# Kernel optimization log

Measured on AMD Instinct MI355X. Metric: run time of the kernel, lower is better.

The kernel has to match this reference:

```python
import jax, jax.numpy as jnp
import numpy as np
from jax import lax

# LNS semantics: values are held as (sign, log_base|x|); exact conversion round-trips
# make log-domain mul/add mathematically identical to float conv/linear/relu, so the
# faithful reference is the equivalent float pipeline.

def _conv(x, w, b):
    # x: [B,C,H,W], w: [O,C,kh,kw] (torch layout), stride 1, no padding
    y = lax.conv_general_dilated(x, w, window_strides=(1, 1), padding='VALID',
                                 dimension_numbers=('NCHW', 'OIHW', 'NCHW'))
    return y + b[None, :, None, None]

def _maxpool2(x):
    return lax.reduce_window(x, -jnp.inf, lax.max,
                             window_dimensions=(1, 1, 2, 2),
                             window_strides=(1, 1, 2, 2), padding='VALID')

def setup_inputs() -> dict:
    key = jax.random.key(0)
    ks = jax.random.split(key, 9)
    s = lambda k, shape, fan: jax.random.normal(k, shape, jnp.float32) * (1.0 / np.sqrt(fan))
    return {
        'x': jax.random.normal(ks[0], (512, 1, 54, 54), jnp.float32),
        'conv1_w': s(ks[1], (32, 1, 3, 3), 9),
        'conv1_b': s(ks[2], (32,), 9),
        'conv2_w': s(ks[3], (64, 32, 3, 3), 32 * 9),
        'conv2_b': s(ks[4], (64,), 32 * 9),
        'fc1_w': s(ks[5], (128, 9216), 9216),
        'fc1_b': s(ks[6], (128,), 9216),
        'fc2_w': s(ks[7], (10, 128), 128),
        'fc2_b': s(ks[8], (10,), 128),
    }

def reference(x, conv1_w, conv1_b, conv2_w, conv2_b, fc1_w, fc1_b, fc2_w, fc2_b):
    h = jnp.maximum(_conv(x, conv1_w, conv1_b), 0.0)          # [B,32,52,52]
    h = _maxpool2(h)                                          # [B,32,26,26]
    h = jnp.maximum(_conv(h, conv2_w, conv2_b), 0.0)          # [B,64,24,24]
    h = _maxpool2(h)                                          # [B,64,12,12]
    h = h.reshape(h.shape[0], -1)                             # [B,9216]
    h = jnp.maximum(h @ fc1_w.T + fc1_b, 0.0)                 # [B,128]
    return h @ fc2_w.T + fc2_b                                # [B,10]
```

## Files before the change

### kernel.cpp

```cpp
#include <hip/hip_runtime.h>


#define B 512
#define POS 676
#define ICP 36
#define P2SZ (64*12*12)
#define SCR 26
#define IMS 58
#define IMCOPY (54 * IMS)
#define PL_USH (POS * ICP)
#define SCRATCH_USH 6656

typedef unsigned short ushort_t;
typedef ushort_t ushort4v __attribute__((ext_vector_type(4)));
typedef _Float16 f16x8 __attribute__((ext_vector_type(8)));
typedef float f32x4 __attribute__((ext_vector_type(4)));

__device__ __forceinline__ ushort_t f2h(float f) {
    union { _Float16 h; ushort_t u; } a; a.h = (_Float16)f; return a.u;
}
__device__ __forceinline__ float h2f(ushort_t u) {
    union { ushort_t u; _Float16 h; } a; a.u = u; return (float)a.h;
}

#define N_WR (64 * 9 * 32)
#define WR_BLOCKS 72
#define TR_BLOCKS 128
#define PREP_THREADS ((WR_BLOCKS + TR_BLOCKS) * 256)

__global__ __launch_bounds__(256) void prep(const float* __restrict__ c2w,
                                            const float* __restrict__ f1w,
                                            ushort_t* __restrict__ wr,
                                            ushort_t* __restrict__ wfb,
                                            float* __restrict__ C) {
    __shared__ float tr[64 * 145];
    int blk = blockIdx.x;
    int tid = threadIdx.x;

    int gtid = blk * 256 + tid;
    for (int i = gtid; i < 512 * 128; i += PREP_THREADS) C[i] = 0.0f;

    if (blk < WR_BLOCKS) {
        int t = blk * 256 + tid;
        int ic  = t & 31;
        int tap = (t >> 5) % 9;
        int oc  = t / 288;
        wr[t] = f2h(c2w[oc * 288 + ic * 9 + tap]);
        return;
    }
    int n = blk - WR_BLOCKS;
    const float* src = f1w + (size_t)n * 9216;
#pragma unroll
    for (int i = 0; i < 36; ++i) {
        int idx = i * 256 + tid;
        int oc = idx / 144, pos = idx - oc * 144;
        tr[oc * 145 + pos] = src[idx];
    }
    __syncthreads();
    ushort_t* dst = wfb + (size_t)n * 9216;
#pragma unroll
    for (int i = 0; i < 36; ++i) {
        int idx = i * 256 + tid;
        int pos = idx >> 6, oc = idx & 63;
        dst[idx] = f2h(tr[oc * 145 + pos]);
    }
}

__global__ __launch_bounds__(512, 4) void conv12(const float* __restrict__ x,
                                                 const float* __restrict__ w1,
                                                 const float* __restrict__ bias1,
                                                 const ushort_t* __restrict__ wr,
                                                 const float* __restrict__ bias2,
                                                 ushort_t* __restrict__ pool2cl) {
    __shared__ ushort_t smem[PL_USH + SCRATCH_USH];
    ushort_t* pl  = smem;
    ushort_t* img = smem + PL_USH;

    int b   = blockIdx.x;
    int tid = threadIdx.x;
    int lane = tid & 63, wid = tid >> 6;
    int quad = lane >> 4, lr = lane & 15;

    for (int i = tid; i < 54; i += 512) {
        ushort_t* r0 = img + i * IMS;
        r0[54] = 0; r0[55] = 0; r0[56] = 0; r0[57] = 0;
        ushort_t* r1 = img + IMCOPY + i * IMS;
        r1[53] = 0; r1[54] = 0; r1[55] = 0; r1[56] = 0; r1[57] = 0;
    }
    if (tid < 96) img[2 * IMCOPY + tid] = 0;

    const float* xim = x + (size_t)b * 2916;
    for (int i = tid; i < 729; i += 512) {
        int e = i * 4;
        int r = e / 54, c = e - r * 54;
        float4 xv = *reinterpret_cast<const float4*>(&xim[e]);
        ushort_t h0 = f2h(xv.x), h1 = f2h(xv.y), h2 = f2h(xv.z), h3 = f2h(xv.w);
        if (c <= 50) {
            ushort_t* p0 = &img[r * IMS + c];
            p0[0] = h0; p0[1] = h1; p0[2] = h2; p0[3] = h3;
            ushort_t* p1 = &img[IMCOPY + r * IMS + c - 1];
            if (c > 0) p1[0] = h0;
            p1[1] = h1; p1[2] = h2; p1[3] = h3;
        } else {
            img[r * IMS + 52] = h0;
            img[r * IMS + 53] = h1;
            img[(r + 1) * IMS + 0] = h2;
            img[(r + 1) * IMS + 1] = h3;
            img[IMCOPY + r * IMS + 51] = h0;
            img[IMCOPY + r * IMS + 52] = h1;
            img[IMCOPY + (r + 1) * IMS + 0] = h3;
        }
    }

    f16x8 bfrag[2];
#pragma unroll
    for (int n = 0; n < 2; ++n) {
        union { ushort_t u[8]; f16x8 v; } bu;
#pragma unroll
        for (int j = 0; j < 8; ++j) bu.u[j] = 0;
        if (quad < 3) {
            const float* wp = w1 + (n * 16 + lr) * 9 + quad * 3;
            bu.u[0] = f2h(wp[0]);
            bu.u[1] = f2h(wp[1]);
            bu.u[2] = f2h(wp[2]);
        }
        bfrag[n] = bu.v;
    }
    float bv0 = bias1[lr], bv1 = bias1[16 + lr];

    __syncthreads();

    int cbase = (lr & 1) ? (IMCOPY + lr - 1) : lr;

    for (int it = 0; it < 4; ++it) {
        int py = wid + it * 8;
        if (py >= 26) break;
        int y0 = 2 * py;
#pragma unroll
        for (int t = 0; t < 4; ++t) {
            int x0 = t * 16;
            int off0 = cbase + x0 + (y0 + quad) * IMS;
            int off1 = off0 + IMS;
            union { unsigned d[4]; f16x8 v; } a0, a1;
            a0.d[0] = *reinterpret_cast<const unsigned*>(&img[off0]);
            a0.d[1] = *reinterpret_cast<const unsigned*>(&img[off0 + 2]);
            a0.d[2] = a0.d[0]; a0.d[3] = a0.d[1];
            a1.d[0] = *reinterpret_cast<const unsigned*>(&img[off1]);
            a1.d[1] = *reinterpret_cast<const unsigned*>(&img[off1 + 2]);
            a1.d[2] = a1.d[0]; a1.d[3] = a1.d[1];

            f32x4 cA0 = (f32x4){0.f,0.f,0.f,0.f}, cA1 = cA0, cB0 = cA0, cB1 = cA0;
            cA0 = __builtin_amdgcn_mfma_f32_16x16x32_f16(a0.v, bfrag[0], cA0, 0, 0, 0);
            cA1 = __builtin_amdgcn_mfma_f32_16x16x32_f16(a0.v, bfrag[1], cA1, 0, 0, 0);
            cB0 = __builtin_amdgcn_mfma_f32_16x16x32_f16(a1.v, bfrag[0], cB0, 0, 0, 0);
            cB1 = __builtin_amdgcn_mfma_f32_16x16x32_f16(a1.v, bfrag[1], cB1, 0, 0, 0);

            if (t < 3 || quad == 0) {
                int px0 = t * 8 + quad * 2;
                float u0 = fmaxf(fmaxf(cA0[0], cA0[1]), fmaxf(cB0[0], cB0[1]));
                float u1 = fmaxf(fmaxf(cA0[2], cA0[3]), fmaxf(cB0[2], cB0[3]));
                float v0 = fmaxf(fmaxf(cA1[0], cA1[1]), fmaxf(cB1[0], cB1[1]));
                float v1 = fmaxf(fmaxf(cA1[2], cA1[3]), fmaxf(cB1[2], cB1[3]));
                ushort_t* po = pl + (py * 26 + px0) * ICP;
                po[lr]            = f2h(fmaxf(u0 + bv0, 0.0f));
                po[16 + lr]       = f2h(fmaxf(v0 + bv1, 0.0f));
                po[ICP + lr]      = f2h(fmaxf(u1 + bv0, 0.0f));
                po[ICP + 16 + lr] = f2h(fmaxf(v1 + bv1, 0.0f));
            }
        }
    }

    __syncthreads();

    int prow  = wid >> 1;
    int nhalf = wid & 1;
    const ushort_t* wb = wr + (size_t)(nhalf * 32 + lr) * 288 + quad * 8;

    int ocl = lane & 31;
    int pxh = lane >> 5;
    int oc  = nhalf * 32 + ocl;
    float bv = bias2[oc];
    ushort_t* scr = smem + PL_USH + wid * (32 * SCR);

    for (int cc = 0; cc < 3; ++cc) {
        int ebase[3];
#pragma unroll
        for (int t = 0; t < 3; ++t) {
            int m  = t * 16 + lr;
            int yl = m / 24;
            int xx = m - yl * 24;
            ebase[t] = ((8 * cc + 2 * prow + yl) * 26 + xx) * ICP + quad * 8;
        }

        f32x4 acc[3][2];
#pragma unroll
        for (int t = 0; t < 3; ++t)
#pragma unroll
            for (int n = 0; n < 2; ++n) acc[t][n] = (f32x4){0.f, 0.f, 0.f, 0.f};

#pragma unroll
        for (int tap = 0; tap < 9; ++tap) {
            int ky = tap / 3, kx = tap % 3;
            int koff = (ky * 26 + kx) * ICP;
            f16x8 a[3];
#pragma unroll
            for (int t = 0; t < 3; ++t) {
                union { ushort4v s[2]; f16x8 v; } u;
                u.s[0] = *reinterpret_cast<const ushort4v*>(&pl[ebase[t] + koff]);
                u.s[1] = *reinterpret_cast<const ushort4v*>(&pl[ebase[t] + koff + 4]);
                a[t] = u.v;
            }
            f16x8 bf[2];
#pragma unroll
            for (int n = 0; n < 2; ++n)
                bf[n] = *reinterpret_cast<const f16x8*>(wb + (size_t)n * 16 * 288 + tap * 32);
#pragma unroll
            for (int t = 0; t < 3; ++t)
#pragma unroll
                for (int n = 0; n < 2; ++n)
                    acc[t][n] = __builtin_amdgcn_mfma_f32_16x16x32_f16(a[t], bf[n], acc[t][n], 0, 0, 0);
        }

#pragma unroll
        for (int t = 0; t < 3; ++t)
#pragma unroll
            for (int n = 0; n < 2; ++n) {
                int wocl = n * 16 + lr;
                int i0 = t * 8 + quad * 2;
                float v0 = fmaxf(acc[t][n][0], acc[t][n][1]);
                float v1 = fmaxf(acc[t][n][2], acc[t][n][3]);
                union { ushort_t u2[2]; unsigned w; } pk;
                pk.u2[0] = f2h(v0); pk.u2[1] = f2h(v1);
                *reinterpret_cast<unsigned*>(&scr[wocl * SCR + i0]) = pk.w;
            }
        asm volatile("s_waitcnt lgkmcnt(0)" ::: "memory");

        const ushort_t* row = scr + ocl * SCR;
        int py = cc * 4 + prow;
        ushort_t* po = pool2cl + ((size_t)b * 144 + py * 12) * 64 + oc;
#pragma unroll
        for (int j = 0; j < 6; ++j) {
            int px = pxh * 6 + j;
            float r0 = h2f(row[px]);
            float r1 = h2f(row[px + 12]);
            po[px * 64] = f2h(fmaxf(fmaxf(r0, r1) + bv, 0.0f));
        }
        asm volatile("s_waitcnt lgkmcnt(0)" ::: "memory");
    }
}

__global__ __launch_bounds__(256) void fc1_mfma(const ushort_t* __restrict__ A,
                                                 const ushort_t* __restrict__ W,
                                                 float* __restrict__ C) {
    int tid = threadIdx.x;
    int lane = tid & 63, wid = tid >> 6;
    int lr = lane & 15, quad = lane >> 4;
    int w  = blockIdx.x * 4 + wid;
    int nt = w & 3;
    int ks = (w >> 2) & 15;
    int mt = w >> 6;

    int m0 = mt * 16;
    int n0 = nt * 32;
    int k0 = ks * 576 + quad * 8;
    const ushort_t* a0 = A + (size_t)(m0 + lr) * 9216 + k0;
    const ushort_t* b0 = W + (size_t)(n0 + lr) * 9216 + k0;
    const ushort_t* b1 = b0 + (size_t)16 * 9216;

    f32x4 acc0 = (f32x4){0.f, 0.f, 0.f, 0.f};
    f32x4 acc1 = (f32x4){0.f, 0.f, 0.f, 0.f};

#pragma unroll
    for (int kk = 0; kk < 18; ++kk) {
        f16x8 av  = *reinterpret_cast<const f16x8*>(a0 + kk * 32);
        f16x8 bv0 = *reinterpret_cast<const f16x8*>(b0 + kk * 32);
        f16x8 bv1 = *reinterpret_cast<const f16x8*>(b1 + kk * 32);
        acc0 = __builtin_amdgcn_mfma_f32_16x16x32_f16(av, bv0, acc0, 0, 0, 0);
        acc1 = __builtin_amdgcn_mfma_f32_16x16x32_f16(av, bv1, acc1, 0, 0, 0);
    }

    int crow = m0 + quad * 4;
#pragma unroll
    for (int r = 0; r < 4; ++r) {
        atomicAdd(&C[(size_t)(crow + r) * 128 + n0 + lr],      acc0[r]);
        atomicAdd(&C[(size_t)(crow + r) * 128 + n0 + 16 + lr], acc1[r]);
    }
}

__global__ __launch_bounds__(256) void fc2k(const float* __restrict__ C,
                                            const float* __restrict__ b1,
                                            const float* __restrict__ w2,
                                            const float* __restrict__ b2,
                                            float* __restrict__ out) {
    __shared__ float h[2][128];
    int half = threadIdx.x >> 7;
    int k = threadIdx.x & 127;
    int b = blockIdx.x * 2 + half;
    float s = C[(size_t)b * 128 + k];
    h[half][k] = fmaxf(s + b1[k], 0.0f);
    __syncthreads();
    if (k < 10) {
        const float* wp = w2 + k * 128;
        float acc = 0.f;
#pragma unroll 8
        for (int j = 0; j < 128; ++j) acc += h[half][j] * wp[j];
        out[b * 10 + k] = acc + b2[k];
    }
}

extern "C" void kernel_launch(void* const* d_in, const int* in_sizes, int n_in,
                              void* d_out, int out_size, void* d_ws, size_t ws_size,
                              hipStream_t stream) {
    const float* x       = (const float*)d_in[0];
    const float* conv1_w = (const float*)d_in[1];
    const float* conv1_b = (const float*)d_in[2];
    const float* conv2_w = (const float*)d_in[3];
    const float* conv2_b = (const float*)d_in[4];
    const float* fc1_w   = (const float*)d_in[5];
    const float* fc1_b   = (const float*)d_in[6];
    const float* fc2_w   = (const float*)d_in[7];
    const float* fc2_b   = (const float*)d_in[8];
    float* out = (float*)d_out;

    char* ws = (char*)d_ws;
    ushort_t* wr = (ushort_t*)ws;
    ws += N_WR * sizeof(ushort_t) + 128;
    ushort_t* wfb = (ushort_t*)ws;
    ws += (size_t)128 * 9216 * sizeof(ushort_t) + 128;
    ushort_t* pool2cl = (ushort_t*)ws;
    ws += (size_t)B * P2SZ * sizeof(ushort_t) + 128;
    float* C = (float*)ws;
    ws += (size_t)512 * 128 * sizeof(float) + 128;

    prep<<<WR_BLOCKS + TR_BLOCKS, 256, 0, stream>>>(conv2_w, fc1_w, wr, wfb, C);
    conv12<<<B, 512, 0, stream>>>(x, conv1_w, conv1_b, wr, conv2_b, pool2cl);
    fc1_mfma<<<512, 256, 0, stream>>>(pool2cl, wfb, C);
    fc2k<<<256, 256, 0, stream>>>(C, fc1_b, fc2_w, fc2_b, out);
}
```

Measured before the change: 114.6 us.

## Fuse fc2 into fc1 via last-block counter and widen fc1 M tile

Each fc1 wave now computes a 32x32 output tile with four MFMA accumulators, halving the block count and reusing the weight loads across two row tiles. A global atomic counter, zeroed in prep, detects the last finishing block, which then applies bias and ReLU and computes the fc2 layer for all rows. This removes the separate fc2 kernel launch. The cost is a serial single-block epilogue at the tail and less parallelism in fc1.

```diff
diff --git a/kernel.cpp b/kernel.cpp
--- a/kernel.cpp
+++ b/kernel.cpp
@@ -27,6 +27,7 @@
 #define WR_BLOCKS 72
 #define TR_BLOCKS 128
 #define PREP_THREADS ((WR_BLOCKS + TR_BLOCKS) * 256)
+#define FC1_BLOCKS 256
 
 __global__ __launch_bounds__(256) void prep(const float* __restrict__ c2w,
                                             const float* __restrict__ f1w,
@@ -38,7 +39,7 @@
     int tid = threadIdx.x;
 
     int gtid = blk * 256 + tid;
-    for (int i = gtid; i < 512 * 128; i += PREP_THREADS) C[i] = 0.0f;
+    for (int i = gtid; i < 512 * 128 + 16; i += PREP_THREADS) C[i] = 0.0f;
 
     if (blk < WR_BLOCKS) {
         int t = blk * 256 + tid;
@@ -250,8 +251,15 @@
 }
 
 __global__ __launch_bounds__(256) void fc1_mfma(const ushort_t* __restrict__ A,
-                                                 const ushort_t* __restrict__ W,
-                                                 float* __restrict__ C) {
+                                                const ushort_t* __restrict__ W,
+                                                float* __restrict__ C,
+                                                int* __restrict__ counter,
+                                                const float* __restrict__ fb1,
+                                                const float* __restrict__ w2,
+                                                const float* __restrict__ fb2,
+                                                float* __restrict__ out) {
+    __shared__ float w2s[10 * 128];
+    __shared__ int lastFlag;
     int tid = threadIdx.x;
     int lane = tid & 63, wid = tid >> 6;
     int lr = lane & 15, quad = lane >> 4;
@@ -260,51 +268,68 @@
     int ks = (w >> 2) & 15;
     int mt = w >> 6;
 
-    int m0 = mt * 16;
+    int m0 = mt * 32;
     int n0 = nt * 32;
     int k0 = ks * 576 + quad * 8;
-    const ushort_t* a0 = A + (size_t)(m0 + lr) * 9216 + k0;
-    const ushort_t* b0 = W + (size_t)(n0 + lr) * 9216 + k0;
-    const ushort_t* b1 = b0 + (size_t)16 * 9216;
-
-    f32x4 acc0 = (f32x4){0.f, 0.f, 0.f, 0.f};
-    f32x4 acc1 = (f32x4){0.f, 0.f, 0.f, 0.f};
+    const ushort_t* a0  = A + (size_t)(m0 + lr) * 9216 + k0;
+    const ushort_t* a1  = a0 + (size_t)16 * 9216;
+    const ushort_t* b0  = W + (size_t)(n0 + lr) * 9216 + k0;
+    const ushort_t* b1p = b0 + (size_t)16 * 9216;
+
+    f32x4 acc00 = (f32x4){0.f,0.f,0.f,0.f};
+    f32x4 acc01 = acc00, acc10 = acc00, acc11 = acc00;
 
 #pragma unroll
     for (int kk = 0; kk < 18; ++kk) {
-        f16x8 av  = *reinterpret_cast<const f16x8*>(a0 + kk * 32);
+        f16x8 av0 = *reinterpret_cast<const f16x8*>(a0 + kk * 32);
+        f16x8 av1 = *reinterpret_cast<const f16x8*>(a1 + kk * 32);
         f16x8 bv0 = *reinterpret_cast<const f16x8*>(b0 + kk * 32);
-        f16x8 bv1 = *reinterpret_cast<const f16x8*>(b1 + kk * 32);
-        acc0 = __builtin_amdgcn_mfma_f32_16x16x32_f16(av, bv0, acc0, 0, 0, 0);
-        acc1 = __builtin_amdgcn_mfma_f32_16x16x32_f16(av, bv1, acc1, 0, 0, 0);
+        f16x8 bv1 = *reinterpret_cast<const f16x8*>(b1p + kk * 32);
+        acc00 = __builtin_amdgcn_mfma_f32_16x16x32_f16(av0, bv0, acc00, 0, 0, 0);
+        acc01 = __builtin_amdgcn_mfma_f32_16x16x32_f16(av0, bv1, acc01, 0, 0, 0);
+        acc10 = __builtin_amdgcn_mfma_f32_16x16x32_f16(av1, bv0, acc10, 0, 0, 0);
+        acc11 = __builtin_amdgcn_mfma_f32_16x16x32_f16(av1, bv1, acc11, 0, 0, 0);
     }
 
     int crow = m0 + quad * 4;
 #pragma unroll
     for (int r = 0; r < 4; ++r) {
-        atomicAdd(&C[(size_t)(crow + r) * 128 + n0 + lr],      acc0[r]);
-        atomicAdd(&C[(size_t)(crow + r) * 128 + n0 + 16 + lr], acc1[r]);
-    }
-}
-
-__global__ __launch_bounds__(256) void fc2k(const float* __restrict__ C,
-                                            const float* __restrict__ b1,
-                                            const float* __restrict__ w2,
-                                            const float* __restrict__ b2,
-                                            float* __restrict__ out) {
-    __shared__ float h[2][128];
-    int half = threadIdx.x >> 7;
-    int k = threadIdx.x & 127;
-    int b = blockIdx.x * 2 + half;
-    float s = C[(size_t)b * 128 + k];
-    h[half][k] = fmaxf(s + b1[k], 0.0f);
-    __syncthreads();
-    if (k < 10) {
-        const float* wp = w2 + k * 128;
-        float acc = 0.f;
-#pragma unroll 8
-        for (int j = 0; j < 128; ++j) acc += h[half][j] * wp[j];
-        out[b * 10 + k] = acc + b2[k];
+        atomicAdd(&C[(size_t)(crow + r) * 128 + n0 + lr],           acc00[r]);
+        atomicAdd(&C[(size_t)(crow + r) * 128 + n0 + 16 + lr],      acc01[r]);
+        atomicAdd(&C[(size_t)(crow + r + 16) * 128 + n0 + lr],      acc10[r]);
+        atomicAdd(&C[(size_t)(crow + r + 16) * 128 + n0 + 16 + lr], acc11[r]);
+    }
+
+    __threadfence();
+    __syncthreads();
+    if (tid == 0) lastFlag = (atomicAdd(counter, 1) == FC1_BLOCKS - 1);
+    __syncthreads();
+    if (!lastFlag) return;
+
+    for (int i = tid; i < 1280; i += 256) w2s[i] = w2[i];
+    __syncthreads();
+
+    float bb2[10];
+#pragma unroll
+    for (int o = 0; o < 10; ++o) bb2[o] = fb2[o];
+
+#pragma unroll
+    for (int rr = 0; rr < 2; ++rr) {
+        int r = tid * 2 + rr;
+        float acc[10];
+#pragma unroll
+        for (int o = 0; o < 10; ++o) acc[o] = 0.f;
+        const float* crowp = C + (size_t)r * 128;
+#pragma unroll 4
+        for (int j = 0; j < 128; ++j) {
+            float cv = __hip_atomic_load(&crowp[j], __ATOMIC_RELAXED,
+                                         __HIP_MEMORY_SCOPE_AGENT);
+            float hv = fmaxf(cv + fb1[j], 0.0f);
+#pragma unroll
+            for (int o = 0; o < 10; ++o) acc[o] += hv * w2s[o * 128 + j];
+        }
+#pragma unroll
+        for (int o = 0; o < 10; ++o) out[r * 10 + o] = acc[o] + bb2[o];
     }
 }
 
@@ -330,10 +355,11 @@
     ushort_t* pool2cl = (ushort_t*)ws;
     ws += (size_t)B * P2SZ * sizeof(ushort_t) + 128;
     float* C = (float*)ws;
-    ws += (size_t)512 * 128 * sizeof(float) + 128;
+    int* counter = (int*)(C + 512 * 128);
+    ws += ((size_t)512 * 128 + 16) * sizeof(float) + 128;
 
     prep<<<WR_BLOCKS + TR_BLOCKS, 256, 0, stream>>>(conv2_w, fc1_w, wr, wfb, C);
     conv12<<<B, 512, 0, stream>>>(x, conv1_w, conv1_b, wr, conv2_b, pool2cl);
-    fc1_mfma<<<512, 256, 0, stream>>>(pool2cl, wfb, C);
-    fc2k<<<256, 256, 0, stream>>>(C, fc1_b, fc2_w, fc2_b, out);
-}
+    fc1_mfma<<<FC1_BLOCKS, 256, 0, stream>>>(pool2cl, wfb, C, counter,
+                                             fc1_b, fc2_w, fc2_b, out);
+}
```

After: 155.7 us. +35.8%, slower.
